# Optimization experiments

Hardware: AMD Instinct MI355X
Metric: run time of the kernel (lower is better)

The kernel has to match this reference:

```python
import jax, jax.numpy as jnp
import numpy as np

# mamba-130m dims (n_layers reduced to 4 for single-device tractability)
B, L, D, DI, N, R, K, V, NL = 2, 512, 768, 1536, 16, 48, 4, 50280, 4


def setup_inputs() -> dict:
    key = jax.random.key(0)
    ks = jax.random.split(key, 10)
    s = 0.02
    return {
        "question_ids": jax.random.randint(ks[0], (B, L), 0, V, dtype=jnp.int32),
        "question_mask": jnp.ones((B, L), dtype=jnp.int32),
        "answer_ids": jax.random.randint(ks[1], (B, L), 0, V, dtype=jnp.int32),
        "answer_mask": jnp.ones((B, L), dtype=jnp.int32),
        "embed": jax.random.normal(ks[2], (V, D), jnp.float32) * s,
        "in_proj_w": jax.random.normal(ks[3], (NL, D, 2 * DI), jnp.float32) * s,
        "conv_w": jax.random.normal(ks[4], (NL, DI, K), jnp.float32) * s,
        "conv_b": jnp.zeros((NL, DI), jnp.float32),
        "x_proj_w": jax.random.normal(ks[5], (NL, DI, R + 2 * N), jnp.float32) * s,
        "dt_proj_w": jax.random.normal(ks[6], (NL, R, DI), jnp.float32) * s,
        # bias ~ -4.6 so softplus(dt) ~ 0.01, like mamba's dt init range
        "dt_proj_b": jnp.full((NL, DI), -4.6, jnp.float32),
        "A_log": jnp.broadcast_to(jnp.log(jnp.arange(1, N + 1, dtype=jnp.float32)), (NL, DI, N)) + jnp.zeros((NL, DI, N), jnp.float32),
        "D_param": jnp.ones((NL, DI), jnp.float32),
        "out_proj_w": jax.random.normal(ks[7], (NL, DI, D), jnp.float32) * s,
        "norm_w": jnp.ones((NL, D), jnp.float32),
        "norm_f_w": jnp.ones((D,), jnp.float32),
    }


def _rms(x, w, eps=1e-5):
    return x * jax.lax.rsqrt(jnp.mean(x * x, axis=-1, keepdims=True) + eps) * w


def _selective_scan(dA, dBu, Ct):
    # dA, dBu: (B, L, DI, N); Ct: (B, L, N)
    def step(h, xs):
        a, b = xs
        h = a * h + b
        return h, h

    h0 = jnp.zeros((dA.shape[0], dA.shape[2], dA.shape[3]), dA.dtype)  # (B, DI, N)
    _, hs = jax.lax.scan(step, h0, (jnp.swapaxes(dA, 0, 1), jnp.swapaxes(dBu, 0, 1)))
    hs = jnp.swapaxes(hs, 0, 1)  # (B, L, DI, N)
    return jnp.einsum('bldn,bln->bld', hs, Ct)


def _block(x, p):
    ipw, cw, cb, xpw, dtw, dtb, Alog, Dp, opw, nw = p
    h = _rms(x, nw)
    xz = h @ ipw                      # (B, L, 2*DI)
    u, z = xz[..., :DI], xz[..., DI:]
    # depthwise causal conv, kernel K
    up = jnp.pad(u, ((0, 0), (K - 1, 0), (0, 0)))
    uc = sum(up[:, k:k + u.shape[1], :] * cw[:, k] for k in range(K)) + cb
    uc = jax.nn.silu(uc)
    proj = uc @ xpw                   # (B, L, R+2N)
    dt = jax.nn.softplus(proj[..., :R] @ dtw + dtb)
    Bt = proj[..., R:R + N]
    Ct = proj[..., R + N:]
    A = -jnp.exp(Alog)                # (DI, N)
    dA = jnp.exp(dt[..., None] * A)   # (B, L, DI, N)
    dBu = (dt * uc)[..., None] * Bt[:, :, None, :]
    y = _selective_scan(dA, dBu, Ct) + uc * Dp
    y = y * jax.nn.silu(z)
    return x + y @ opw


def _lm_loss(ids, mask, embed, layers, norm_f_w):
    x = embed[ids] * mask[..., None].astype(embed.dtype)
    for p in layers:
        x = _block(x, p)
    x = _rms(x, norm_f_w)
    logits = x @ embed.T              # tied lm head, (B, L, V)
    logp = jax.nn.log_softmax(logits[:, :-1], axis=-1)
    lbl = ids[:, 1:]
    nll = -jnp.take_along_axis(logp, lbl[..., None], axis=-1)[..., 0]
    m = mask[:, 1:].astype(logp.dtype)
    return jnp.sum(nll * m) / jnp.maximum(jnp.sum(m), 1.0)


def reference(question_ids, question_mask, answer_ids, answer_mask, embed, in_proj_w, conv_w, conv_b, x_proj_w, dt_proj_w, dt_proj_b, A_log, D_param, out_proj_w, norm_w, norm_f_w):
    layers = [
        (in_proj_w[l], conv_w[l], conv_b[l], x_proj_w[l], dt_proj_w[l], dt_proj_b[l], A_log[l], D_param[l], out_proj_w[l], norm_w[l])
        for l in range(NL)
    ]
    loss_q = _lm_loss(question_ids, question_mask, embed, layers, norm_f_w)
    loss_a = _lm_loss(answer_ids, answer_mask, embed, layers, norm_f_w)
    return loss_a + loss_q
```

## Files before the change

### kernel.cpp

```cpp
#include <hip/hip_runtime.h>
#include <hip/hip_bf16.h>
#include <cstdint>
#include <cstddef>

#define T_TOK   2048
#define DM      768
#define DI      1536
#define NST     16
#define RRANK   48
#define KCONV   4
#define VOCAB   50280
#define NLAYER  4
#define SEQL    512
#define NTILE_V 197
#define NCHUNK  8
#define CHL     64

typedef __bf16 bf16x8 __attribute__((ext_vector_type(8)));
typedef float  f32x4  __attribute__((ext_vector_type(4)));

__device__ inline unsigned short f2b(float f) {
  union { float f; unsigned u; } v; v.f = f;
  unsigned r = v.u + 0x7FFFu + ((v.u >> 16) & 1u);
  return (unsigned short)(r >> 16);
}
__device__ inline float b2f(unsigned short h) {
  union { unsigned u; float f; } v; v.u = ((unsigned)h) << 16;
  return v.f;
}

__device__ inline void gload_lds16(const unsigned short* g, unsigned short* l) {
  __builtin_amdgcn_global_load_lds(
      (const __attribute__((address_space(1))) void*)g,
      (__attribute__((address_space(3))) void*)l, 16, 0, 0);
}

__global__ __launch_bounds__(256) void transpose_conv_kernel(
    const float* __restrict__ src, unsigned short* __restrict__ dst,
    int R, int C, int Rpad) {
  __shared__ float tile[32][33];
  const float* s = src + (size_t)blockIdx.z * R * C;
  unsigned short* d = dst + (size_t)blockIdx.z * C * Rpad;
  int c0 = blockIdx.x * 32, r0 = blockIdx.y * 32;
  int tx = threadIdx.x & 31, ty = threadIdx.x >> 5;
  #pragma unroll
  for (int i = 0; i < 32; i += 8) {
    int r = r0 + ty + i, c = c0 + tx;
    tile[ty + i][tx] = (r < R && c < C) ? s[(size_t)r * C + c] : 0.f;
  }
  __syncthreads();
  #pragma unroll
  for (int i = 0; i < 32; i += 8) {
    int c = c0 + ty + i, r = r0 + tx;
    if (c < C && r < Rpad) d[(size_t)c * Rpad + r] = f2b(tile[tx][ty + i]);
  }
}

__global__ __launch_bounds__(256) void cvt_embed_kernel(
    const float* __restrict__ e, unsigned short* __restrict__ eb) {
  const int n4 = VOCAB * DM / 4;
  for (int i = blockIdx.x * 256 + threadIdx.x; i < n4; i += gridDim.x * 256) {
    float4 f = *(const float4*)(e + (size_t)i * 4);
    union { unsigned long long u; unsigned short h[4]; } pk;
    pk.h[0] = f2b(f.x); pk.h[1] = f2b(f.y); pk.h[2] = f2b(f.z); pk.h[3] = f2b(f.w);
    *(unsigned long long*)(eb + (size_t)i * 4) = pk.u;
  }
}

__global__ __launch_bounds__(256) void gather_kernel(
    const int* __restrict__ qids, const int* __restrict__ qmask,
    const int* __restrict__ aids, const int* __restrict__ amask,
    const float* __restrict__ embed, float* __restrict__ x) {
  int idx = blockIdx.x * 256 + threadIdx.x;
  int t = idx / DM, d = idx - t * DM;
  int seq = t >> 9, pos = t & 511;
  const int* ids = (seq < 2) ? qids : aids;
  const int* msk = (seq < 2) ? qmask : amask;
  int s2 = seq & 1;
  int id = ids[s2 * SEQL + pos];
  float m = (float)msk[s2 * SEQL + pos];
  x[idx] = embed[(size_t)id * DM + d] * m;
}

__global__ __launch_bounds__(256) void rmsnorm_kernel(
    const float* __restrict__ x, const float* __restrict__ w,
    unsigned short* __restrict__ h) {
  int t = blockIdx.x;
  const float* xr = x + (size_t)t * DM;
  float ss = 0.f;
  for (int d = threadIdx.x; d < DM; d += 256) { float v = xr[d]; ss += v * v; }
  for (int o = 1; o < 64; o <<= 1) ss += __shfl_xor(ss, o);
  __shared__ float wsum[4];
  if ((threadIdx.x & 63) == 0) wsum[threadIdx.x >> 6] = ss;
  __syncthreads();
  ss = wsum[0] + wsum[1] + wsum[2] + wsum[3];
  float sc = rsqrtf(ss / (float)DM + 1e-5f);
  for (int d = threadIdx.x; d < DM; d += 256)
    h[(size_t)t * DM + d] = f2b(xr[d] * sc * w[d]);
}

__global__ __launch_bounds__(256) void resid_rms_kernel(
    float* __restrict__ x, const float* __restrict__ part,
    const float* __restrict__ w, unsigned short* __restrict__ h) {
  int t = blockIdx.x;
  float v[3];
  float ss = 0.f;
  #pragma unroll
  for (int j = 0; j < 3; ++j) {
    int d = threadIdx.x + j * 256;
    size_t o = (size_t)t * DM + d;
    float xv = x[o] + part[o] + part[(size_t)T_TOK * DM + o] +
               part[(size_t)2 * T_TOK * DM + o] + part[(size_t)3 * T_TOK * DM + o];
    x[o] = xv; v[j] = xv; ss += xv * xv;
  }
  for (int o = 1; o < 64; o <<= 1) ss += __shfl_xor(ss, o);
  __shared__ float wsum[4];
  if ((threadIdx.x & 63) == 0) wsum[threadIdx.x >> 6] = ss;
  __syncthreads();
  ss = wsum[0] + wsum[1] + wsum[2] + wsum[3];
  float sc = rsqrtf(ss / (float)DM + 1e-5f);
  #pragma unroll
  for (int j = 0; j < 3; ++j) {
    int d = threadIdx.x + j * 256;
    h[(size_t)t * DM + d] = f2b(v[j] * sc * w[d]);
  }
}

template <int EPI>
__global__ __launch_bounds__(256) void gemm_bf16_kernel(
    const unsigned short* __restrict__ A, int lda,
    const unsigned short* __restrict__ B, int ldb,
    float* __restrict__ C, unsigned short* __restrict__ Cbf,
    float* __restrict__ CT, int ldc,
    const float* __restrict__ bias,
    int M, int N, int K, int mtiles) {
  __shared__ __attribute__((aligned(16))) unsigned short As[128 * 64];
  __shared__ __attribute__((aligned(16))) unsigned short Bs[128 * 64];
  int bid = blockIdx.x;
  int m0 = (bid % mtiles) * 128;
  int rest = bid / mtiles;
  int n0, split = 0;
  int ntil = (N + 127) >> 7;
  if (EPI == 6) { split = rest / ntil; n0 = (rest % ntil) * 128; }
  else n0 = rest * 128;
  const unsigned short* Ap = (EPI == 6) ? A + (size_t)split * K : A;
  const unsigned short* Bp = (EPI == 6) ? B + (size_t)split * K : B;
  int tid = threadIdx.x;
  int lane = tid & 63, w = tid >> 6;
  int wr = w >> 1, wc = w & 1;
  f32x4 acc[4][4] = {};

  int lrow = lane >> 3;
  int lcol = (((lane & 7) ^ (lrow & 7)) & 7) * 8;
  auto STAGE = [&](int k0) {
    #pragma unroll
    for (int it = 0; it < 4; ++it) {
      int r = w * 32 + it * 8;
      gload_lds16(Ap + (size_t)(m0 + r + lrow) * lda + k0 + lcol, &As[r * 64]);
      int br = n0 + r + lrow; if (br > N - 1) br = N - 1;
      gload_lds16(Bp + (size_t)br * ldb + k0 + lcol, &Bs[r * 64]);
    }
  };

  int nst = K / 64;
  int rA = wr * 64 + (lane & 15);
  int rB = wc * 64 + (lane & 15);
  int sw = lane & 7, ckb = lane >> 4;
  for (int s = 0; s < nst; ++s) {
    STAGE(s * 64);
    __syncthreads();
    __builtin_amdgcn_s_setprio(1);
    #pragma unroll
    for (int ks = 0; ks < 2; ++ks) {
      int ca = (((ks * 4 + ckb) ^ sw) & 7) * 8;
      bf16x8 a[4], b[4];
      #pragma unroll
      for (int i = 0; i < 4; ++i) a[i] = *(const bf16x8*)(&As[(rA + i * 16) * 64 + ca]);
      #pragma unroll
      for (int i = 0; i < 4; ++i) b[i] = *(const bf16x8*)(&Bs[(rB + i * 16) * 64 + ca]);
      #pragma unroll
      for (int mi = 0; mi < 4; ++mi)
        #pragma unroll
        for (int ni = 0; ni < 4; ++ni)
          acc[mi][ni] = __builtin_amdgcn_mfma_f32_16x16x32_bf16(a[mi], b[ni], acc[mi][ni], 0, 0, 0);
    }
    __builtin_amdgcn_s_setprio(0);
    __syncthreads();
  }

  int g = lane >> 4, c = lane & 15;
  #pragma unroll
  for (int mi = 0; mi < 4; ++mi)
    #pragma unroll
    for (int ni = 0; ni < 4; ++ni) {
      int col = n0 + wc * 64 + ni * 16 + c;
      int row0 = m0 + wr * 64 + mi * 16 + g * 4;
      if (col < N) {
        if (EPI == 5) {
          float4 o;
          float* ov = (float*)&o;
          #pragma unroll
          for (int r = 0; r < 4; ++r) {
            float xv = acc[mi][ni][r] + bias[col];
            ov[r] = (xv > 20.f) ? xv : log1pf(__expf(xv));
          }
          *(float4*)(&CT[(size_t)col * T_TOK + row0]) = o;
        } else if (EPI == 7) {
          if (col < DI) {
            #pragma unroll
            for (int r = 0; r < 4; ++r)
              C[(size_t)(row0 + r) * DI + col] = acc[mi][ni][r];
          } else {
            float4 o;
            float* ov = (float*)&o;
            #pragma unroll
            for (int r = 0; r < 4; ++r) {
              float zv = acc[mi][ni][r];
              ov[r] = zv / (1.f + __expf(-zv));
            }
            *(float4*)(&CT[(size_t)(col - DI) * T_TOK + row0]) = o;
          }
        } else {
          #pragma unroll
          for (int r = 0; r < 4; ++r) {
            int row = row0 + r;
            float v = acc[mi][ni][r];
            if (EPI == 0) C[(size_t)row * ldc + col] = v;
            if (EPI == 1) C[(size_t)row * ldc + col] += v;
            if (EPI == 6) C[((size_t)split * M + row) * ldc + col] = v;
          }
        }
      }
    }
}

__global__ __launch_bounds__(512) void gemm_lse_kernel(
    const unsigned short* __restrict__ A,
    const unsigned short* __restrict__ B,
    float* __restrict__ pmax, float* __restrict__ psum,
    int mtiles) {
  __shared__ __attribute__((aligned(16))) unsigned short As[128 * 64];
  __shared__ __attribute__((aligned(16))) unsigned short Bs[256 * 64];
  __shared__ float lmax[128][4];
  __shared__ float lsum[128][4];
  const int K = DM, Nv = VOCAB;
  int bid = blockIdx.x;
  int m0 = (bid % mtiles) * 128;
  int n0 = (bid / mtiles) * 256;
  int tid = threadIdx.x;
  int lane = tid & 63, w = tid >> 6;
  int wr = w >> 2, wc = w & 3;
  f32x4 acc[4][4] = {};

  int lrow = lane >> 3;
  int lcol = (((lane & 7) ^ (lrow & 7)) & 7) * 8;
  auto STAGE = [&](int k0) {
    #pragma unroll
    for (int it = 0; it < 2; ++it) {
      int r = w * 16 + it * 8;
      gload_lds16(A + (size_t)(m0 + r + lrow) * K + k0 + lcol, &As[r * 64]);
    }
    #pragma unroll
    for (int it = 0; it < 4; ++it) {
      int r = w * 32 + it * 8;
      int br = n0 + r + lrow; if (br > Nv - 1) br = Nv - 1;
      gload_lds16(B + (size_t)br * K + k0 + lcol, &Bs[r * 64]);
    }
  };

  const int nst = K / 64;
  int rA = wr * 64 + (lane & 15);
  int rB = wc * 64 + (lane & 15);
  int sw = lane & 7, ckb = lane >> 4;
  for (int s = 0; s < nst; ++s) {
    STAGE(s * 64);
    __syncthreads();
    __builtin_amdgcn_s_setprio(1);
    #pragma unroll
    for (int ks = 0; ks < 2; ++ks) {
      int ca = (((ks * 4 + ckb) ^ sw) & 7) * 8;
      bf16x8 a[4], b[4];
      #pragma unroll
      for (int i = 0; i < 4; ++i) a[i] = *(const bf16x8*)(&As[(rA + i * 16) * 64 + ca]);
      #pragma unroll
      for (int i = 0; i < 4; ++i) b[i] = *(const bf16x8*)(&Bs[(rB + i * 16) * 64 + ca]);
      #pragma unroll
      for (int mi = 0; mi < 4; ++mi)
        #pragma unroll
        for (int ni = 0; ni < 4; ++ni)
          acc[mi][ni] = __builtin_amdgcn_mfma_f32_16x16x32_bf16(a[mi], b[ni], acc[mi][ni], 0, 0, 0);
    }
    __builtin_amdgcn_s_setprio(0);
    __syncthreads();
  }

  int g = lane >> 4, c = lane & 15;
  #pragma unroll
  for (int mi = 0; mi < 4; ++mi) {
    #pragma unroll
    for (int r = 0; r < 4; ++r) {
      float mx = -INFINITY;
      #pragma unroll
      for (int ni = 0; ni < 4; ++ni) {
        int col = n0 + wc * 64 + ni * 16 + c;
        float v = (col < Nv) ? acc[mi][ni][r] : -INFINITY;
        mx = fmaxf(mx, v);
      }
      mx = fmaxf(mx, __shfl_xor(mx, 1, 16));
      mx = fmaxf(mx, __shfl_xor(mx, 2, 16));
      mx = fmaxf(mx, __shfl_xor(mx, 4, 16));
      mx = fmaxf(mx, __shfl_xor(mx, 8, 16));
      float ssum = 0.f;
      #pragma unroll
      for (int ni = 0; ni < 4; ++ni) {
        int col = n0 + wc * 64 + ni * 16 + c;
        if (col < Nv) ssum += __expf(acc[mi][ni][r] - mx);
      }
      ssum += __shfl_xor(ssum, 1, 16);
      ssum += __shfl_xor(ssum, 2, 16);
      ssum += __shfl_xor(ssum, 4, 16);
      ssum += __shfl_xor(ssum, 8, 16);
      if (c == 0) {
        int rl = wr * 64 + mi * 16 + g * 4 + r;
        lmax[rl][wc] = mx;
        lsum[rl][wc] = ssum;
      }
    }
  }
  __syncthreads();
  if (tid < 128) {
    float m0v = lmax[tid][0], m1 = lmax[tid][1], m2 = lmax[tid][2], m3 = lmax[tid][3];
    float Mx = fmaxf(fmaxf(m0v, m1), fmaxf(m2, m3));
    float S = lsum[tid][0] * __expf(m0v - Mx) + lsum[tid][1] * __expf(m1 - Mx) +
              lsum[tid][2] * __expf(m2 - Mx) + lsum[tid][3] * __expf(m3 - Mx);
    int row = m0 + tid;
    int nb = n0 >> 8;
    pmax[(size_t)row * NTILE_V + nb] = Mx;
    psum[(size_t)row * NTILE_V + nb] = S;
  }
}

__global__ __launch_bounds__(256) void xproj_reduce_kernel(
    const float* __restrict__ part, unsigned short* __restrict__ projbf,
    float* __restrict__ BCt) {
  int idx = blockIdx.x * 256 + threadIdx.x;
  int row = idx / 80, col = idx - row * 80;
  float v = part[idx] + part[(size_t)T_TOK * 80 + idx] +
            part[(size_t)2 * T_TOK * 80 + idx] + part[(size_t)3 * T_TOK * 80 + idx];
  projbf[idx] = f2b(v);
  if (col >= RRANK) BCt[(size_t)(col - RRANK) * T_TOK + row] = v;
}

__global__ __launch_bounds__(256) void conv_silu_kernel(
    const float* __restrict__ ur, const float* __restrict__ cw,
    const float* __restrict__ cb,
    unsigned short* __restrict__ ucbf, float* __restrict__ ucT) {
  __shared__ float xu[67][64];
  __shared__ float ou[64][65];
  int t0 = blockIdx.x * 64;
  int ch0 = blockIdx.y * 64;
  int tid = threadIdx.x;
  int cx = tid & 63, ty = tid >> 6;
  bool seq_start = (t0 & 511) == 0;
  for (int r = ty; r < 67; r += 4) {
    int tg = t0 - 3 + r;
    float v = 0.f;
    if (r >= 3 || !seq_start) v = ur[(size_t)tg * DI + ch0 + cx];
    xu[r][cx] = v;
  }
  __syncthreads();
  int ch = ch0 + cx;
  float4 wv = *(const float4*)(cw + ch * 4);
  float bias = cb[ch];
  #pragma unroll
  for (int i = 0; i < 16; ++i) {
    int tr = ty * 16 + i;
    float a = bias + xu[tr][cx] * wv.x + xu[tr + 1][cx] * wv.y +
              xu[tr + 2][cx] * wv.z + xu[tr + 3][cx] * wv.w;
    float s = a / (1.f + __expf(-a));
    ucbf[(size_t)(t0 + tr) * DI + ch] = f2b(s);
    ou[tr][cx] = s;
  }
  __syncthreads();
  int tx = tid & 63, cy = tid >> 6;
  #pragma unroll
  for (int i = 0; i < 16; ++i) {
    int chi = cy * 16 + i;
    ucT[(size_t)(ch0 + chi) * T_TOK + t0 + tx] = ou[tx][chi];
  }
}

__global__ __launch_bounds__(256) void scan_sum_kernel(
    const float* __restrict__ dtT, const float* __restrict__ ucT,
    const float* __restrict__ BCt, const float* __restrict__ Alog,
    float* __restrict__ Pbuf, float* __restrict__ Fbuf) {
  int bc = blockIdx.x / 96;
  int idx = (blockIdx.x % 96) * 256 + threadIdx.x;
  int n = idx & 15, d = idx >> 4;
  int b = bc >> 3, chunk = bc & 7;
  float A = -__expf(Alog[d * NST + n]);
  int t0 = b * SEQL + chunk * CHL;
  const float4* dp = (const float4*)(dtT + (size_t)d * T_TOK + t0);
  const float4* up = (const float4*)(ucT + (size_t)d * T_TOK + t0);
  const float4* Bp = (const float4*)(BCt + (size_t)n * T_TOK + t0);
  float h = 0.f, sdt = 0.f;
  #pragma unroll
  for (int q = 0; q < CHL / 4; ++q) {
    float4 d4 = dp[q], u4 = up[q], B4 = Bp[q];
    float a;
    a = __expf(d4.x * A); h = fmaf(a, h, d4.x * u4.x * B4.x);
    a = __expf(d4.y * A); h = fmaf(a, h, d4.y * u4.y * B4.y);
    a = __expf(d4.z * A); h = fmaf(a, h, d4.z * u4.z * B4.z);
    a = __expf(d4.w * A); h = fmaf(a, h, d4.w * u4.w * B4.w);
    sdt += d4.x + d4.y + d4.z + d4.w;
  }
  size_t s = ((size_t)bc * DI + d) * NST + n;
  Pbuf[s] = __expf(A * sdt);
  Fbuf[s] = h;
}

__global__ __launch_bounds__(256) void scan_emit_kernel(
    const float* __restrict__ dtT, const float* __restrict__ ucT,
    const float* __restrict__ BCt, const float* __restrict__ zsT,
    const float* __restrict__ Alog, const float* __restrict__ Dpar,
    const float* __restrict__ Pbuf, const float* __restrict__ Fbuf,
    unsigned short* __restrict__ yg) {
  int bc = blockIdx.x / 96;
  int idx = (blockIdx.x % 96) * 256 + threadIdx.x;
  int n = idx & 15, d = idx >> 4;
  int b = bc >> 3, chunk = bc & 7;
  float A = -__expf(Alog[d * NST + n]);
  float Dpv = Dpar[d];
  float h = 0.f;
  for (int j = 0; j < chunk; ++j) {
    size_t s = (((size_t)(b * NCHUNK + j)) * DI + d) * NST + n;
    h = Fbuf[s] + Pbuf[s] * h;
  }
  int t0 = b * SEQL + chunk * CHL;
  const float4* dp = (const float4*)(dtT + (size_t)d * T_TOK + t0);
  const float4* up = (const float4*)(ucT + (size_t)d * T_TOK + t0);
  const float4* Bp = (const float4*)(BCt + (size_t)n * T_TOK + t0);
  const float4* Cp = (const float4*)(BCt + (size_t)(NST + n) * T_TOK + t0);
  const float4* zp = (const float4*)(zsT + (size_t)d * T_TOK + t0);
  unsigned short* yp = yg + (size_t)t0 * DI + d;
  #pragma unroll 4
  for (int q = 0; q < CHL / 4; ++q) {
    float4 d4 = dp[q], u4 = up[q], B4 = Bp[q], C4 = Cp[q], z4 = zp[q];
    float y0, y1, y2, y3, a, cc;
    a = __expf(d4.x * A); h = fmaf(a, h, d4.x * u4.x * B4.x); cc = h * C4.x;
    cc += __shfl_xor(cc, 1, 16); cc += __shfl_xor(cc, 2, 16);
    cc += __shfl_xor(cc, 4, 16); cc += __shfl_xor(cc, 8, 16);
    y0 = (cc + u4.x * Dpv) * z4.x;
    a = __expf(d4.y * A); h = fmaf(a, h, d4.y * u4.y * B4.y); cc = h * C4.y;
    cc += __shfl_xor(cc, 1, 16); cc += __shfl_xor(cc, 2, 16);
    cc += __shfl_xor(cc, 4, 16); cc += __shfl_xor(cc, 8, 16);
    y1 = (cc + u4.y * Dpv) * z4.y;
    a = __expf(d4.z * A); h = fmaf(a, h, d4.z * u4.z * B4.z); cc = h * C4.z;
    cc += __shfl_xor(cc, 1, 16); cc += __shfl_xor(cc, 2, 16);
    cc += __shfl_xor(cc, 4, 16); cc += __shfl_xor(cc, 8, 16);
    y2 = (cc + u4.z * Dpv) * z4.z;
    a = __expf(d4.w * A); h = fmaf(a, h, d4.w * u4.w * B4.w); cc = h * C4.w;
    cc += __shfl_xor(cc, 1, 16); cc += __shfl_xor(cc, 2, 16);
    cc += __shfl_xor(cc, 4, 16); cc += __shfl_xor(cc, 8, 16);
    y3 = (cc + u4.w * Dpv) * z4.w;
    if (n == 0) {
      yp[(size_t)(q * 4 + 0) * DI] = f2b(y0);
      yp[(size_t)(q * 4 + 1) * DI] = f2b(y1);
      yp[(size_t)(q * 4 + 2) * DI] = f2b(y2);
      yp[(size_t)(q * 4 + 3) * DI] = f2b(y3);
    }
  }
}

__global__ __launch_bounds__(64) void lse_reduce_kernel(
    const float* __restrict__ pmax, const float* __restrict__ psum,
    float* __restrict__ lse) {
  int row = blockIdx.x;
  int lane = threadIdx.x;
  const float* pm = pmax + (size_t)row * NTILE_V;
  const float* ps = psum + (size_t)row * NTILE_V;
  float m = -INFINITY;
  for (int j = lane; j < NTILE_V; j += 64) m = fmaxf(m, pm[j]);
  for (int o = 1; o < 64; o <<= 1) m = fmaxf(m, __shfl_xor(m, o));
  float s = 0.f;
  for (int j = lane; j < NTILE_V; j += 64) s += ps[j] * __expf(pm[j] - m);
  for (int o = 1; o < 64; o <<= 1) s += __shfl_xor(s, o);
  if (lane == 0) lse[row] = m + __logf(s);
}

__global__ __launch_bounds__(256) void label_dot_kernel(
    const unsigned short* __restrict__ h, const unsigned short* __restrict__ eb,
    const int* __restrict__ qids, const int* __restrict__ aids,
    float* __restrict__ ldot) {
  int row = blockIdx.x * 4 + (threadIdx.x >> 6);
  int lane = threadIdx.x & 63;
  int pos = row & 511, seq = row >> 9;
  if (pos == 511) { if (lane == 0) ldot[row] = 0.f; return; }
  const int* ids = (seq < 2) ? qids : aids;
  int lbl = ids[(seq & 1) * SEQL + pos + 1];
  const unsigned short* hr = h + (size_t)row * DM;
  const unsigned short* er = eb + (size_t)lbl * DM;
  float s = 0.f;
  for (int k = lane; k < DM; k += 64) s += b2f(hr[k]) * b2f(er[k]);
  for (int o = 1; o < 64; o <<= 1) s += __shfl_xor(s, o);
  if (lane == 0) ldot[row] = s;
}

__global__ __launch_bounds__(256) void loss_kernel(
    const float* __restrict__ lse, const float* __restrict__ ldot,
    const int* __restrict__ qmask, const int* __restrict__ amask,
    float* __restrict__ out) {
  float nq = 0.f, dq = 0.f, na = 0.f, da = 0.f;
  for (int row = threadIdx.x; row < T_TOK; row += 256) {
    int pos = row & 511, seq = row >> 9;
    if (pos == 511) continue;
    const int* msk = (seq < 2) ? qmask : amask;
    float m = (float)msk[(seq & 1) * SEQL + pos + 1];
    float nll = (lse[row] - ldot[row]) * m;
    if (seq < 2) { nq += nll; dq += m; } else { na += nll; da += m; }
  }
  for (int o = 1; o < 64; o <<= 1) {
    nq += __shfl_xor(nq, o); dq += __shfl_xor(dq, o);
    na += __shfl_xor(na, o); da += __shfl_xor(da, o);
  }
  __shared__ float red[4][4];
  int w = threadIdx.x >> 6;
  if ((threadIdx.x & 63) == 0) { red[w][0] = nq; red[w][1] = dq; red[w][2] = na; red[w][3] = da; }
  __syncthreads();
  if (threadIdx.x == 0) {
    nq = 0.f; dq = 0.f; na = 0.f; da = 0.f;
    for (int i = 0; i < 4; ++i) { nq += red[i][0]; dq += red[i][1]; na += red[i][2]; da += red[i][3]; }
    float lq = nq / fmaxf(dq, 1.f);
    float la = na / fmaxf(da, 1.f);
    out[0] = lq + la;
  }
}

extern "C" void kernel_launch(void* const* d_in, const int* in_sizes, int n_in,
                              void* d_out, int out_size, void* d_ws, size_t ws_size,
                              hipStream_t stream) {
  const int*   qids  = (const int*)d_in[0];
  const int*   qmask = (const int*)d_in[1];
  const int*   aids  = (const int*)d_in[2];
  const int*   amask = (const int*)d_in[3];
  const float* embed = (const float*)d_in[4];
  const float* ipw   = (const float*)d_in[5];
  const float* cw    = (const float*)d_in[6];
  const float* cb    = (const float*)d_in[7];
  const float* xpw   = (const float*)d_in[8];
  const float* dtw   = (const float*)d_in[9];
  const float* dtb   = (const float*)d_in[10];
  const float* Alog  = (const float*)d_in[11];
  const float* Dp    = (const float*)d_in[12];
  const float* opw   = (const float*)d_in[13];
  const float* nw    = (const float*)d_in[14];
  const float* nfw   = (const float*)d_in[15];

  char* wp = (char*)d_ws;
  auto alloc = [&](size_t bytes) { char* p = wp; wp += (bytes + 255) & ~(size_t)255; return p; };

  float*          x      = (float*)alloc((size_t)T_TOK * DM * 4);
  unsigned short* hbf    = (unsigned short*)alloc((size_t)T_TOK * DM * 2);
  float*          ur     = (float*)alloc((size_t)T_TOK * DI * 4);
  unsigned short* ucbf   = (unsigned short*)alloc((size_t)T_TOK * DI * 2);
  unsigned short* projbf = (unsigned short*)alloc((size_t)T_TOK * 80 * 2);
  unsigned short* ygbf   = (unsigned short*)alloc((size_t)T_TOK * DI * 2);
  float*          ucT    = (float*)alloc((size_t)DI * T_TOK * 4);
  float*          zsT    = (float*)alloc((size_t)DI * T_TOK * 4);
  float*          dtT    = (float*)alloc((size_t)DI * T_TOK * 4);
  float*          BCt    = (float*)alloc((size_t)2 * NST * T_TOK * 4);
  float*          Pbuf   = (float*)alloc((size_t)4 * NCHUNK * DI * NST * 4);
  float*          Fbuf   = (float*)alloc((size_t)4 * NCHUNK * DI * NST * 4);
  float*          xpart  = (float*)alloc((size_t)4 * T_TOK * 80 * 4);
  float*          opart  = (float*)alloc((size_t)4 * T_TOK * DM * 4);
  unsigned short* ipw_t  = (unsigned short*)alloc((size_t)NLAYER * 2 * DI * DM * 2);
  unsigned short* opw_t  = (unsigned short*)alloc((size_t)NLAYER * DM * DI * 2);
  unsigned short* xpw_t  = (unsigned short*)alloc((size_t)NLAYER * 80 * DI * 2);
  unsigned short* dtw_t  = (unsigned short*)alloc((size_t)NLAYER * DI * 64 * 2);
  unsigned short* embbf  = (unsigned short*)alloc((size_t)VOCAB * DM * 2);
  float*          pmax   = (float*)alloc((size_t)T_TOK * NTILE_V * 4);
  float*          psum   = (float*)alloc((size_t)T_TOK * NTILE_V * 4);
  float*          lseb   = (float*)alloc((size_t)T_TOK * 4);
  float*          ldot   = (float*)alloc((size_t)T_TOK * 4);

  transpose_conv_kernel<<<dim3(96, 24, NLAYER), 256, 0, stream>>>(ipw, ipw_t, DM, 2 * DI, DM);
  transpose_conv_kernel<<<dim3(24, 48, NLAYER), 256, 0, stream>>>(opw, opw_t, DI, DM, DI);
  transpose_conv_kernel<<<dim3(3, 48, NLAYER), 256, 0, stream>>>(xpw, xpw_t, DI, 80, DI);
  transpose_conv_kernel<<<dim3(48, 2, NLAYER), 256, 0, stream>>>(dtw, dtw_t, RRANK, DI, 64);
  cvt_embed_kernel<<<2048, 256, 0, stream>>>(embed, embbf);

  gather_kernel<<<(T_TOK * DM) / 256, 256, 0, stream>>>(qids, qmask, aids, amask, embed, x);
  rmsnorm_kernel<<<T_TOK, 256, 0, stream>>>(x, nw, hbf);

  const int mt = T_TOK / 128;
  for (int l = 0; l < NLAYER; ++l) {
    gemm_bf16_kernel<7><<<mt * (2 * DI / 128), 256, 0, stream>>>(
        hbf, DM, ipw_t + (size_t)l * 2 * DI * DM, DM, ur, nullptr, zsT, DI,
        nullptr, T_TOK, 2 * DI, DM, mt);
    conv_silu_kernel<<<dim3(T_TOK / 64, DI / 64), 256, 0, stream>>>(
        ur, cw + (size_t)l * DI * KCONV, cb + (size_t)l * DI, ucbf, ucT);
    gemm_bf16_kernel<6><<<mt * 1 * 4, 256, 0, stream>>>(
        ucbf, DI, xpw_t + (size_t)l * 80 * DI, DI, xpart, nullptr, nullptr, 80,
        nullptr, T_TOK, 80, DI / 4, mt);
    xproj_reduce_kernel<<<(T_TOK * 80) / 256, 256, 0, stream>>>(xpart, projbf, BCt);
    gemm_bf16_kernel<5><<<mt * (DI / 128), 256, 0, stream>>>(
        projbf, 80, dtw_t + (size_t)l * DI * 64, 64, nullptr, nullptr, dtT, DI,
        dtb + (size_t)l * DI, T_TOK, DI, 64, mt);
    scan_sum_kernel<<<32 * 96, 256, 0, stream>>>(
        dtT, ucT, BCt, Alog + (size_t)l * DI * NST, Pbuf, Fbuf);
    scan_emit_kernel<<<32 * 96, 256, 0, stream>>>(
        dtT, ucT, BCt, zsT, Alog + (size_t)l * DI * NST, Dp + (size_t)l * DI,
        Pbuf, Fbuf, ygbf);
    gemm_bf16_kernel<6><<<mt * (DM / 128) * 4, 256, 0, stream>>>(
        ygbf, DI, opw_t + (size_t)l * DM * DI, DI, opart, nullptr, nullptr, DM,
        nullptr, T_TOK, DM, DI / 4, mt);
    resid_rms_kernel<<<T_TOK, 256, 0, stream>>>(
        x, opart, (l < NLAYER - 1) ? (nw + (l + 1) * DM) : nfw, hbf);
  }

  gemm_lse_kernel<<<mt * NTILE_V, 512, 0, stream>>>(hbf, embbf, pmax, psum, mt);
  lse_reduce_kernel<<<T_TOK, 64, 0, stream>>>(pmax, psum, lseb);
  label_dot_kernel<<<T_TOK / 4, 256, 0, stream>>>(hbf, embbf, qids, aids, ldot);
  loss_kernel<<<1, 256, 0, stream>>>(lseb, ldot, qmask, amask, (float*)d_out);
}
```

Baseline: 1.119 ms.

## Fold dt_proj into x_proj weights and widen in_proj GEMM tiles

```diff
diff --git a/kernel.cpp b/kernel.cpp
--- a/kernel.cpp
+++ b/kernel.cpp
@@ -15,6 +15,7 @@
 #define NTILE_V 197
 #define NCHUNK  8
 #define CHL     64
+#define NCAT    1568
 
 typedef __bf16 bf16x8 __attribute__((ext_vector_type(8)));
 typedef float  f32x4  __attribute__((ext_vector_type(4)));
@@ -67,36 +68,82 @@
   }
 }
 
-__global__ __launch_bounds__(256) void gather_kernel(
+__global__ __launch_bounds__(256) void wcat_bc_kernel(
+    const float* __restrict__ xpw, unsigned short* __restrict__ wcat) {
+  int l = blockIdx.y;
+  int idx = blockIdx.x * 256 + threadIdx.x;
+  int n = idx / DI, k = idx - n * DI;
+  wcat[(size_t)l * NCAT * DI + (size_t)n * DI + k] =
+      f2b(xpw[(size_t)l * DI * 80 + (size_t)k * 80 + 48 + n]);
+}
+
+__global__ __launch_bounds__(256) void wdt_kernel(
+    const float* __restrict__ xpw, const float* __restrict__ dtw,
+    unsigned short* __restrict__ wcat) {
+  __shared__ float xs[64][49];
+  __shared__ float ds[48][64];
+  int l = blockIdx.z;
+  int k0 = blockIdx.x * 64, n0 = blockIdx.y * 64;
+  const float* xp = xpw + (size_t)l * DI * 80;
+  const float* dp = dtw + (size_t)l * RRANK * DI;
+  int tid = threadIdx.x;
+  {
+    int row = tid >> 2, cg = (tid & 3) * 12;
+    #pragma unroll
+    for (int c = 0; c < 12; ++c)
+      xs[row][cg + c] = xp[(size_t)(k0 + row) * 80 + cg + c];
+    int col = tid & 63, rb = tid >> 6;
+    #pragma unroll
+    for (int i = 0; i < 12; ++i)
+      ds[rb + 4 * i][col] = dp[(size_t)(rb + 4 * i) * DI + n0 + col];
+  }
+  __syncthreads();
+  int tx = tid & 63, ty = tid >> 6;
+  float acc[16] = {};
+  #pragma unroll 8
+  for (int r = 0; r < 48; ++r) {
+    float xv = xs[tx][r];
+    #pragma unroll
+    for (int i = 0; i < 16; ++i) acc[i] += xv * ds[r][ty + 4 * i];
+  }
+  unsigned short* wl = wcat + (size_t)l * NCAT * DI + (size_t)(32 + n0) * DI;
+  #pragma unroll
+  for (int i = 0; i < 16; ++i)
+    wl[(size_t)(ty + 4 * i) * DI + k0 + tx] = f2b(acc[i]);
+}
+
+__global__ __launch_bounds__(256) void gather_rms_kernel(
     const int* __restrict__ qids, const int* __restrict__ qmask,
     const int* __restrict__ aids, const int* __restrict__ amask,
-    const float* __restrict__ embed, float* __restrict__ x) {
-  int idx = blockIdx.x * 256 + threadIdx.x;
-  int t = idx / DM, d = idx - t * DM;
+    const float* __restrict__ embed, const float* __restrict__ w,
+    float* __restrict__ x, unsigned short* __restrict__ h) {
+  int t = blockIdx.x;
   int seq = t >> 9, pos = t & 511;
   const int* ids = (seq < 2) ? qids : aids;
   const int* msk = (seq < 2) ? qmask : amask;
   int s2 = seq & 1;
   int id = ids[s2 * SEQL + pos];
   float m = (float)msk[s2 * SEQL + pos];
-  x[idx] = embed[(size_t)id * DM + d] * m;
-}
-
-__global__ __launch_bounds__(256) void rmsnorm_kernel(
-    const float* __restrict__ x, const float* __restrict__ w,
-    unsigned short* __restrict__ h) {
-  int t = blockIdx.x;
-  const float* xr = x + (size_t)t * DM;
-  float ss = 0.f;
-  for (int d = threadIdx.x; d < DM; d += 256) { float v = xr[d]; ss += v * v; }
+  const float* er = embed + (size_t)id * DM;
+  float v[3], ss = 0.f;
+  #pragma unroll
+  for (int j = 0; j < 3; ++j) {
+    int d = threadIdx.x + j * 256;
+    float vv = er[d] * m;
+    x[(size_t)t * DM + d] = vv;
+    v[j] = vv; ss += vv * vv;
+  }
   for (int o = 1; o < 64; o <<= 1) ss += __shfl_xor(ss, o);
   __shared__ float wsum[4];
   if ((threadIdx.x & 63) == 0) wsum[threadIdx.x >> 6] = ss;
   __syncthreads();
   ss = wsum[0] + wsum[1] + wsum[2] + wsum[3];
   float sc = rsqrtf(ss / (float)DM + 1e-5f);
-  for (int d = threadIdx.x; d < DM; d += 256)
-    h[(size_t)t * DM + d] = f2b(xr[d] * sc * w[d]);
+  #pragma unroll
+  for (int j = 0; j < 3; ++j) {
+    int d = threadIdx.x + j * 256;
+    h[(size_t)t * DM + d] = f2b(v[j] * sc * w[d]);
+  }
 }
 
 __global__ __launch_bounds__(256) void resid_rms_kernel(
@@ -130,21 +177,18 @@
 __global__ __launch_bounds__(256) void gemm_bf16_kernel(
     const unsigned short* __restrict__ A, int lda,
     const unsigned short* __restrict__ B, int ldb,
-    float* __restrict__ C, unsigned short* __restrict__ Cbf,
-    float* __restrict__ CT, int ldc,
-    const float* __restrict__ bias,
+    float* __restrict__ C, int ldc,
     int M, int N, int K, int mtiles) {
   __shared__ __attribute__((aligned(16))) unsigned short As[128 * 64];
   __shared__ __attribute__((aligned(16))) unsigned short Bs[128 * 64];
   int bid = blockIdx.x;
   int m0 = (bid % mtiles) * 128;
   int rest = bid / mtiles;
-  int n0, split = 0;
   int ntil = (N + 127) >> 7;
-  if (EPI == 6) { split = rest / ntil; n0 = (rest % ntil) * 128; }
-  else n0 = rest * 128;
-  const unsigned short* Ap = (EPI == 6) ? A + (size_t)split * K : A;
-  const unsigned short* Bp = (EPI == 6) ? B + (size_t)split * K : B;
+  int split = rest / ntil;
+  int n0 = (rest % ntil) * 128;
+  const unsigned short* Ap = A + (size_t)split * K;
+  const unsigned short* Bp = B + (size_t)split * K;
   int tid = threadIdx.x;
   int lane = tid & 63, w = tid >> 6;
   int wr = w >> 1, wc = w & 1;
@@ -196,39 +240,108 @@
       int col = n0 + wc * 64 + ni * 16 + c;
       int row0 = m0 + wr * 64 + mi * 16 + g * 4;
       if (col < N) {
-        if (EPI == 5) {
-          float4 o;
-          float* ov = (float*)&o;
+        #pragma unroll
+        for (int r = 0; r < 4; ++r)
+          C[((size_t)split * M + row0 + r) * ldc + col] = acc[mi][ni][r];
+      }
+    }
+}
+
+template <int EPI>
+__global__ __launch_bounds__(512) void gemm_wide_kernel(
+    const unsigned short* __restrict__ A, int lda,
+    const unsigned short* __restrict__ B, int ldb,
+    float* __restrict__ O1, float* __restrict__ OT,
+    const float* __restrict__ bias,
+    int N, int K, int mtiles) {
+  __shared__ __attribute__((aligned(16))) unsigned short As[128 * 64];
+  __shared__ __attribute__((aligned(16))) unsigned short Bs[256 * 64];
+  int bid = blockIdx.x;
+  int m0 = (bid % mtiles) * 128;
+  int n0 = (bid / mtiles) * 256;
+  int tid = threadIdx.x;
+  int lane = tid & 63, w = tid >> 6;
+  int wr = w >> 2, wc = w & 3;
+  f32x4 acc[4][4] = {};
+
+  int lrow = lane >> 3;
+  int lcol = (((lane & 7) ^ (lrow & 7)) & 7) * 8;
+  auto STAGE = [&](int k0) {
+    #pragma unroll
+    for (int it = 0; it < 2; ++it) {
+      int r = w * 16 + it * 8;
+      gload_lds16(A + (size_t)(m0 + r + lrow) * lda + k0 + lcol, &As[r * 64]);
+    }
+    #pragma unroll
+    for (int it = 0; it < 4; ++it) {
+      int r = w * 32 + it * 8;
+      int br = n0 + r + lrow; if (br > N - 1) br = N - 1;
+      gload_lds16(B + (size_t)br * ldb + k0 + lcol, &Bs[r * 64]);
+    }
+  };
+
+  int nst = K / 64;
+  int rA = wr * 64 + (lane & 15);
+  int rB = wc * 64 + (lane & 15);
+  int sw = lane & 7, ckb = lane >> 4;
+  for (int s = 0; s < nst; ++s) {
+    STAGE(s * 64);
+    __syncthreads();
+    __builtin_amdgcn_s_setprio(1);
+    #pragma unroll
+    for (int ks = 0; ks < 2; ++ks) {
+      int ca = (((ks * 4 + ckb) ^ sw) & 7) * 8;
+      bf16x8 a[4], b[4];
+      #pragma unroll
+      for (int i = 0; i < 4; ++i) a[i] = *(const bf16x8*)(&As[(rA + i * 16) * 64 + ca]);
+      #pragma unroll
+      for (int i = 0; i < 4; ++i) b[i] = *(const bf16x8*)(&Bs[(rB + i * 16) * 64 + ca]);
+      #pragma unroll
+      for (int mi = 0; mi < 4; ++mi)
+        #pragma unroll
+        for (int ni = 0; ni < 4; ++ni)
+          acc[mi][ni] = __builtin_amdgcn_mfma_f32_16x16x32_bf16(a[mi], b[ni], acc[mi][ni], 0, 0, 0);
+    }
+    __builtin_amdgcn_s_setprio(0);
+    __syncthreads();
+  }
+
+  int g = lane >> 4, c = lane & 15;
+  #pragma unroll
+  for (int mi = 0; mi < 4; ++mi)
+    #pragma unroll
+    for (int ni = 0; ni < 4; ++ni) {
+      int col = n0 + wc * 64 + ni * 16 + c;
+      int row0 = m0 + wr * 64 + mi * 16 + g * 4;
+      if (EPI == 7) {
+        if (col < DI) {
+          #pragma unroll
+          for (int r = 0; r < 4; ++r)
+            O1[(size_t)(row0 + r) * DI + col] = acc[mi][ni][r];
+        } else {
+          float4 o; float* ov = (float*)&o;
           #pragma unroll
           for (int r = 0; r < 4; ++r) {
-            float xv = acc[mi][ni][r] + bias[col];
+            float zv = acc[mi][ni][r];
+            ov[r] = zv / (1.f + __expf(-zv));
+          }
+          *(float4*)(&OT[(size_t)(col - DI) * T_TOK + row0]) = o;
+        }
+      }
+      if (EPI == 8) {
+        if (col < 32) {
+          float4 o; float* ov = (float*)&o;
+          #pragma unroll
+          for (int r = 0; r < 4; ++r) ov[r] = acc[mi][ni][r];
+          *(float4*)(&O1[(size_t)col * T_TOK + row0]) = o;
+        } else if (col < NCAT) {
+          float4 o; float* ov = (float*)&o;
+          #pragma unroll
+          for (int r = 0; r < 4; ++r) {
+            float xv = acc[mi][ni][r] + bias[col - 32];
             ov[r] = (xv > 20.f) ? xv : log1pf(__expf(xv));
           }
-          *(float4*)(&CT[(size_t)col * T_TOK + row0]) = o;
-        } else if (EPI == 7) {
-          if (col < DI) {
-            #pragma unroll
-            for (int r = 0; r < 4; ++r)
-              C[(size_t)(row0 + r) * DI + col] = acc[mi][ni][r];
-          } else {
-            float4 o;
-            float* ov = (float*)&o;
-            #pragma unroll
-            for (int r = 0; r < 4; ++r) {
-              float zv = acc[mi][ni][r];
-              ov[r] = zv / (1.f + __expf(-zv));
-            }
-            *(float4*)(&CT[(size_t)(col - DI) * T_TOK + row0]) = o;
-          }
-        } else {
-          #pragma unroll
-          for (int r = 0; r < 4; ++r) {
-            int row = row0 + r;
-            float v = acc[mi][ni][r];
-            if (EPI == 0) C[(size_t)row * ldc + col] = v;
-            if (EPI == 1) C[(size_t)row * ldc + col] += v;
-            if (EPI == 6) C[((size_t)split * M + row) * ldc + col] = v;
-          }
+          *(float4*)(&OT[(size_t)(col - 32) * T_TOK + row0]) = o;
         }
       }
     }
@@ -338,17 +451,6 @@
     pmax[(size_t)row * NTILE_V + nb] = Mx;
     psum[(size_t)row * NTILE_V + nb] = S;
   }
-}
-
-__global__ __launch_bounds__(256) void xproj_reduce_kernel(
-    const float* __restrict__ part, unsigned short* __restrict__ projbf,
-    float* __restrict__ BCt) {
-  int idx = blockIdx.x * 256 + threadIdx.x;
-  int row = idx / 80, col = idx - row * 80;
-  float v = part[idx] + part[(size_t)T_TOK * 80 + idx] +
-            part[(size_t)2 * T_TOK * 80 + idx] + part[(size_t)3 * T_TOK * 80 + idx];
-  projbf[idx] = f2b(v);
-  if (col >= RRANK) BCt[(size_t)(col - RRANK) * T_TOK + row] = v;
 }
 
 __global__ __launch_bounds__(256) void conv_silu_kernel(
@@ -472,11 +574,14 @@
   }
 }
 
-__global__ __launch_bounds__(64) void lse_reduce_kernel(
+__global__ __launch_bounds__(256) void lse_label_kernel(
     const float* __restrict__ pmax, const float* __restrict__ psum,
-    float* __restrict__ lse) {
-  int row = blockIdx.x;
-  int lane = threadIdx.x;
+    const unsigned short* __restrict__ h, const unsigned short* __restrict__ eb,
+    const int* __restrict__ qids, const int* __restrict__ qmask,
+    const int* __restrict__ aids, const int* __restrict__ amask,
+    float* __restrict__ nllm, float* __restrict__ mrow) {
+  int row = blockIdx.x * 4 + (threadIdx.x >> 6);
+  int lane = threadIdx.x & 63;
   const float* pm = pmax + (size_t)row * NTILE_V;
   const float* ps = psum + (size_t)row * NTILE_V;
   float m = -INFINITY;
@@ -485,39 +590,32 @@
   float s = 0.f;
   for (int j = lane; j < NTILE_V; j += 64) s += ps[j] * __expf(pm[j] - m);
   for (int o = 1; o < 64; o <<= 1) s += __shfl_xor(s, o);
-  if (lane == 0) lse[row] = m + __logf(s);
-}
-
-__global__ __launch_bounds__(256) void label_dot_kernel(
-    const unsigned short* __restrict__ h, const unsigned short* __restrict__ eb,
-    const int* __restrict__ qids, const int* __restrict__ aids,
-    float* __restrict__ ldot) {
-  int row = blockIdx.x * 4 + (threadIdx.x >> 6);
-  int lane = threadIdx.x & 63;
+  float lse = m + __logf(s);
   int pos = row & 511, seq = row >> 9;
-  if (pos == 511) { if (lane == 0) ldot[row] = 0.f; return; }
-  const int* ids = (seq < 2) ? qids : aids;
-  int lbl = ids[(seq & 1) * SEQL + pos + 1];
-  const unsigned short* hr = h + (size_t)row * DM;
-  const unsigned short* er = eb + (size_t)lbl * DM;
-  float s = 0.f;
-  for (int k = lane; k < DM; k += 64) s += b2f(hr[k]) * b2f(er[k]);
-  for (int o = 1; o < 64; o <<= 1) s += __shfl_xor(s, o);
-  if (lane == 0) ldot[row] = s;
-}
-
-__global__ __launch_bounds__(256) void loss_kernel(
-    const float* __restrict__ lse, const float* __restrict__ ldot,
-    const int* __restrict__ qmask, const int* __restrict__ amask,
+  float nll = 0.f, mv = 0.f;
+  if (pos != 511) {
+    const int* ids = (seq < 2) ? qids : aids;
+    const int* msk = (seq < 2) ? qmask : amask;
+    int lbl = ids[(seq & 1) * SEQL + pos + 1];
+    mv = (float)msk[(seq & 1) * SEQL + pos + 1];
+    const unsigned short* hr = h + (size_t)row * DM;
+    const unsigned short* er = eb + (size_t)lbl * DM;
+    float dt = 0.f;
+    for (int k = lane; k < DM; k += 64) dt += b2f(hr[k]) * b2f(er[k]);
+    for (int o = 1; o < 64; o <<= 1) dt += __shfl_xor(dt, o);
+    nll = (lse - dt) * mv;
+  }
+  if (lane == 0) { nllm[row] = nll; mrow[row] = mv; }
+}
+
+__global__ __launch_bounds__(256) void loss2_kernel(
+    const float* __restrict__ nllm, const float* __restrict__ mrow,
     float* __restrict__ out) {
   float nq = 0.f, dq = 0.f, na = 0.f, da = 0.f;
   for (int row = threadIdx.x; row < T_TOK; row += 256) {
-    int pos = row & 511, seq = row >> 9;
-    if (pos == 511) continue;
-    const int* msk = (seq < 2) ? qmask : amask;
-    float m = (float)msk[(seq & 1) * SEQL + pos + 1];
-    float nll = (lse[row] - ldot[row]) * m;
-    if (seq < 2) { nq += nll; dq += m; } else { na += nll; da += m; }
+    int seq = row >> 9;
+    if (seq < 2) { nq += nllm[row]; dq += mrow[row]; }
+    else         { na += nllm[row]; da += mrow[row]; }
   }
   for (int o = 1; o < 64; o <<= 1) {
     nq += __shfl_xor(nq, o); dq += __shfl_xor(dq, o);
@@ -563,7 +661,6 @@
   unsigned short* hbf    = (unsigned short*)alloc((size_t)T_TOK * DM * 2);
   float*          ur     = (float*)alloc((size_t)T_TOK * DI * 4);
   unsigned short* ucbf   = (unsigned short*)alloc((size_t)T_TOK * DI * 2);
-  unsigned short* projbf = (unsigned short*)alloc((size_t)T_TOK * 80 * 2);
   unsigned short* ygbf   = (unsigned short*)alloc((size_t)T_TOK * DI * 2);
   float*          ucT    = (float*)alloc((size_t)DI * T_TOK * 4);
   float*          zsT    = (float*)alloc((size_t)DI * T_TOK * 4);
@@ -571,55 +668,48 @@
   float*          BCt    = (float*)alloc((size_t)2 * NST * T_TOK * 4);
   float*          Pbuf   = (float*)alloc((size_t)4 * NCHUNK * DI * NST * 4);
   float*          Fbuf   = (float*)alloc((size_t)4 * NCHUNK * DI * NST * 4);
-  float*          xpart  = (float*)alloc((size_t)4 * T_TOK * 80 * 4);
   float*          opart  = (float*)alloc((size_t)4 * T_TOK * DM * 4);
   unsigned short* ipw_t  = (unsigned short*)alloc((size_t)NLAYER * 2 * DI * DM * 2);
   unsigned short* opw_t  = (unsigned short*)alloc((size_t)NLAYER * DM * DI * 2);
-  unsigned short* xpw_t  = (unsigned short*)alloc((size_t)NLAYER * 80 * DI * 2);
-  unsigned short* dtw_t  = (unsigned short*)alloc((size_t)NLAYER * DI * 64 * 2);
+  unsigned short* wcat   = (unsigned short*)alloc((size_t)NLAYER * NCAT * DI * 2);
   unsigned short* embbf  = (unsigned short*)alloc((size_t)VOCAB * DM * 2);
   float*          pmax   = (float*)alloc((size_t)T_TOK * NTILE_V * 4);
   float*          psum   = (float*)alloc((size_t)T_TOK * NTILE_V * 4);
-  float*          lseb   = (float*)alloc((size_t)T_TOK * 4);
-  float*          ldot   = (float*)alloc((size_t)T_TOK * 4);
+  float*          nllm   = (float*)alloc((size_t)T_TOK * 4);
+  float*          mrow   = (float*)alloc((size_t)T_TOK * 4);
 
   transpose_conv_kernel<<<dim3(96, 24, NLAYER), 256, 0, stream>>>(ipw, ipw_t, DM, 2 * DI, DM);
   transpose_conv_kernel<<<dim3(24, 48, NLAYER), 256, 0, stream>>>(opw, opw_t, DI, DM, DI);
-  transpose_conv_kernel<<<dim3(3, 48, NLAYER), 256, 0, stream>>>(xpw, xpw_t, DI, 80, DI);
-  transpose_conv_kernel<<<dim3(48, 2, NLAYER), 256, 0, stream>>>(dtw, dtw_t, RRANK, DI, 64);
   cvt_embed_kernel<<<2048, 256, 0, stream>>>(embed, embbf);
-
-  gather_kernel<<<(T_TOK * DM) / 256, 256, 0, stream>>>(qids, qmask, aids, amask, embed, x);
-  rmsnorm_kernel<<<T_TOK, 256, 0, stream>>>(x, nw, hbf);
+  wcat_bc_kernel<<<dim3(192, NLAYER), 256, 0, stream>>>(xpw, wcat);
+  wdt_kernel<<<dim3(24, 24, NLAYER), 256, 0, stream>>>(xpw, dtw, wcat);
+
+  gather_rms_kernel<<<T_TOK, 256, 0, stream>>>(qids, qmask, aids, amask, embed, nw, x, hbf);
 
   const int mt = T_TOK / 128;
   for (int l = 0; l < NLAYER; ++l) {
-    gemm_bf16_kernel<7><<<mt * (2 * DI / 128), 256, 0, stream>>>(
-        hbf, DM, ipw_t + (size_t)l * 2 * DI * DM, DM, ur, nullptr, zsT, DI,
-        nullptr, T_TOK, 2 * DI, DM, mt);
+    gemm_wide_kernel<7><<<mt * 12, 512, 0, stream>>>(
+        hbf, DM, ipw_t + (size_t)l * 2 * DI * DM, DM, ur, zsT, nullptr,
+        2 * DI, DM, mt);
     conv_silu_kernel<<<dim3(T_TOK / 64, DI / 64), 256, 0, stream>>>(
         ur, cw + (size_t)l * DI * KCONV, cb + (size_t)l * DI, ucbf, ucT);
-    gemm_bf16_kernel<6><<<mt * 1 * 4, 256, 0, stream>>>(
-        ucbf, DI, xpw_t + (size_t)l * 80 * DI, DI, xpart, nullptr, nullptr, 80,
-        nullptr, T_TOK, 80, DI / 4, mt);
-    xproj_reduce_kernel<<<(T_TOK * 80) / 256, 256, 0, stream>>>(xpart, projbf, BCt);
-    gemm_bf16_kernel<5><<<mt * (DI / 128), 256, 0, stream>>>(
-        projbf, 80, dtw_t + (size_t)l * DI * 64, 64, nullptr, nullptr, dtT, DI,
-        dtb + (size_t)l * DI, T_TOK, DI, 64, mt);
+    gemm_wide_kernel<8><<<mt * 7, 512, 0, stream>>>(
+        ucbf, DI, wcat + (size_t)l * NCAT * DI, DI, BCt, dtT,
+        dtb + (size_t)l * DI, NCAT, DI, mt);
     scan_sum_kernel<<<32 * 96, 256, 0, stream>>>(
         dtT, ucT, BCt, Alog + (size_t)l * DI * NST, Pbuf, Fbuf);
     scan_emit_kernel<<<32 * 96, 256, 0, stream>>>(
         dtT, ucT, BCt, zsT, Alog + (size_t)l * DI * NST, Dp + (size_t)l * DI,
         Pbuf, Fbuf, ygbf);
     gemm_bf16_kernel<6><<<mt * (DM / 128) * 4, 256, 0, stream>>>(
-        ygbf, DI, opw_t + (size_t)l * DM * DI, DI, opart, nullptr, nullptr, DM,
-        nullptr, T_TOK, DM, DI / 4, mt);
+        ygbf, DI, opw_t + (size_t)l * DM * DI, DI, opart, DM,
+        T_TOK, DM, DI / 4, mt);
     resid_rms_kernel<<<T_TOK, 256, 0, stream>>>(
         x, opart, (l < NLAYER - 1) ? (nw + (l + 1) * DM) : nfw, hbf);
   }
 
   gemm_lse_kernel<<<mt * NTILE_V, 512, 0, stream>>>(hbf, embbf, pmax, psum, mt);
-  lse_reduce_kernel<<<T_TOK, 64, 0, stream>>>(pmax, psum, lseb);
-  label_dot_kernel<<<T_TOK / 4, 256, 0, stream>>>(hbf, embbf, qids, aids, ldot);
-  loss_kernel<<<1, 256, 0, stream>>>(lseb, ldot, qmask, amask, (float*)d_out);
-}
+  lse_label_kernel<<<T_TOK / 4, 256, 0, stream>>>(
+      pmax, psum, hbf, embbf, qids, qmask, aids, amask, nllm, mrow);
+  loss2_kernel<<<1, 256, 0, stream>>>(nllm, mrow, (float*)d_out);
+}
```

After: 1.236 ms. +10.4%, slower.
